# Performance work log

Measured on AMD Instinct MI355X. Metric: run time of the kernel, lower is better.

The kernel has to match this reference:

```python
import jax, jax.numpy as jnp
import numpy as np

N_NODES = 100000
N_EDGES = 1600000
F_IN_N = 64
F_IN_E = 64
F_OUT_N = 64
F_OUT_E = 64


def setup_inputs() -> dict:
    key = jax.random.key(0)
    ks = jax.random.split(key, 10)
    nfeats = jax.random.normal(ks[0], (N_NODES, F_IN_N), dtype=jnp.float32)
    efeats = jax.random.normal(ks[1], (N_EDGES, F_IN_E), dtype=jnp.float32)
    src = jax.random.randint(ks[2], (N_EDGES,), 0, N_NODES, dtype=jnp.int32)
    dst = jax.random.randint(ks[3], (N_EDGES,), 0, N_NODES, dtype=jnp.int32)
    s = 0.05
    W_node = jax.random.normal(ks[4], (F_OUT_N, F_IN_N), dtype=jnp.float32) * s
    b_node = jnp.zeros((F_OUT_N,), dtype=jnp.float32)
    W_ni = jax.random.normal(ks[5], (F_OUT_E, F_IN_N), dtype=jnp.float32) * s
    W_nj = jax.random.normal(ks[6], (F_OUT_E, F_IN_N), dtype=jnp.float32) * s
    W_fij = jax.random.normal(ks[7], (F_OUT_E, F_IN_E), dtype=jnp.float32) * s
    bias = jnp.zeros((F_OUT_E,), dtype=jnp.float32)
    return {"nfeats": nfeats, "efeats": efeats, "src": src, "dst": dst,
            "W_node": W_node, "b_node": b_node, "W_ni": W_ni, "W_nj": W_nj,
            "W_fij": W_fij, "bias": bias}


def reference(nfeats, efeats, src, dst, W_node, b_node, W_ni, W_nj, W_fij, bias):
    # edge update: leaky_relu(f_ni[src] + f_nj[dst] + f_fij + bias)
    f_ni = nfeats @ W_ni.T        # [N, Fe]
    f_nj = nfeats @ W_nj.T        # [N, Fe]
    f_fij = efeats @ W_fij.T      # [E, Fe]
    f_out = jax.nn.leaky_relu(f_ni[src] + f_nj[dst] + f_fij + bias, negative_slope=0.01)
    # node update: mean over in-edges of transformed source features
    h = nfeats @ W_node.T + b_node                      # [N, Fn]
    msg_sum = jax.ops.segment_sum(h[src], dst, num_segments=N_NODES)   # [N, Fn]
    deg = jax.ops.segment_sum(jnp.ones((src.shape[0],), dtype=h.dtype), dst,
                              num_segments=N_NODES)
    h_out = msg_sum / jnp.maximum(deg, 1.0)[:, None]    # 0 for isolated nodes
    return (h_out, f_out)
```

## Files before the change

kernel.cpp:

```cpp
#include <hip/hip_runtime.h>

#define NN 100000
#define NE 1600000
#define F 64
#define NSB ((NN + 255) / 256)
#define NTB ((NN + 127) / 128)

typedef float f32x4 __attribute__((ext_vector_type(4)));
typedef float f32x2 __attribute__((ext_vector_type(2)));
typedef short bf16x8 __attribute__((ext_vector_type(8)));

__device__ inline unsigned short f2bf(float f) {
    unsigned u = __builtin_bit_cast(unsigned, f);
    u = (u + 0x7fffu + ((u >> 16) & 1u)) >> 16;
    return (unsigned short)u;
}
__device__ inline float bf2f(unsigned short b) { return __builtin_bit_cast(float, (unsigned)b << 16); }
__device__ inline float bflo(unsigned u) { return __builtin_bit_cast(float, u << 16); }
__device__ inline float bfhi(unsigned u) { return __builtin_bit_cast(float, u & 0xffff0000u); }

__device__ inline bf16x8 pack8(const f32x4 v0, const f32x4 v1) {
    bf16x8 pk;
    pk[0] = (short)f2bf(v0[0]); pk[1] = (short)f2bf(v0[1]);
    pk[2] = (short)f2bf(v0[2]); pk[3] = (short)f2bf(v0[3]);
    pk[4] = (short)f2bf(v1[0]); pk[5] = (short)f2bf(v1[1]);
    pk[6] = (short)f2bf(v1[2]); pk[7] = (short)f2bf(v1[3]);
    return pk;
}

__global__ __launch_bounds__(256, 2) void node_kernel(
    const float* __restrict__ nfeats,
    const float* __restrict__ W_node, const float* __restrict__ b_node,
    const float* __restrict__ W_ni,   const float* __restrict__ W_nj,
    unsigned short* __restrict__ f_ni16, unsigned short* __restrict__ f_nj16,
    unsigned short* __restrict__ h16, int* __restrict__ counts)
{
    __shared__ bf16x8 As8[128 * 8];
    __shared__ bf16x8 Ws8[64 * 8];
    float* Df = reinterpret_cast<float*>(As8);

    const int t = threadIdx.x;
    const int w = t >> 6, lane = t & 63;
    const int tile0 = blockIdx.x * 128;
    const int m = blockIdx.y;

    if (m == 0 && t < 128 && tile0 + t < NN) counts[tile0 + t] = 0;

    {
        const float* Wp = (m == 0) ? W_ni : (m == 1) ? W_nj : W_node;
        const f32x4* gw = reinterpret_cast<const f32x4*>(Wp);
#pragma unroll
        for (int i = 0; i < 2; ++i) {
            const int c = i * 256 + t;
            const int row = c >> 3, slot = c & 7;
            Ws8[row * 8 + (slot ^ (row & 7))] = pack8(gw[2 * c], gw[2 * c + 1]);
        }
    }
    {
        const f32x4* gsrc = reinterpret_cast<const f32x4*>(nfeats + (size_t)tile0 * F);
#pragma unroll
        for (int i = 0; i < 4; ++i) {
            const int c = i * 256 + t;
            const int row = c >> 3, slot = c & 7;
            f32x4 v0 = f32x4{0.f, 0.f, 0.f, 0.f}, v1 = f32x4{0.f, 0.f, 0.f, 0.f};
            if (tile0 + row < NN) { v0 = gsrc[2 * c]; v1 = gsrc[2 * c + 1]; }
            As8[row * 8 + (slot ^ (row & 7))] = pack8(v0, v1);
        }
    }
    __syncthreads();

    bf16x8 af[2][2];
#pragma unroll
    for (int mt = 0; mt < 2; ++mt)
#pragma unroll
        for (int ks = 0; ks < 2; ++ks) {
            const int row = w * 32 + mt * 16 + (lane & 15);
            const int kslot = ks * 4 + (lane >> 4);
            af[mt][ks] = As8[row * 8 + (kslot ^ (row & 7))];
        }

    bf16x8 bfr[4][2];
#pragma unroll
    for (int nt = 0; nt < 4; ++nt)
#pragma unroll
        for (int ks = 0; ks < 2; ++ks) {
            const int c = nt * 16 + (lane & 15);
            const int kslot = ks * 4 + (lane >> 4);
            bfr[nt][ks] = Ws8[c * 8 + (kslot ^ (c & 7))];
        }

    f32x4 acc[2][4];
#pragma unroll
    for (int mt = 0; mt < 2; ++mt)
#pragma unroll
        for (int nt = 0; nt < 4; ++nt) acc[mt][nt] = f32x4{0.f, 0.f, 0.f, 0.f};
#pragma unroll
    for (int ks = 0; ks < 2; ++ks)
#pragma unroll
        for (int mt = 0; mt < 2; ++mt)
#pragma unroll
            for (int nt = 0; nt < 4; ++nt)
                acc[mt][nt] = __builtin_amdgcn_mfma_f32_16x16x32_bf16(
                    af[mt][ks], bfr[nt][ks], acc[mt][nt], 0, 0, 0);

    __syncthreads();

    unsigned short* outp = (m == 0) ? f_ni16 : (m == 1) ? f_nj16 : h16;

#pragma unroll
    for (int half = 0; half < 2; ++half) {
#pragma unroll
        for (int mt = 0; mt < 2; ++mt)
#pragma unroll
            for (int ntl = 0; ntl < 2; ++ntl) {
#pragma unroll
                for (int r = 0; r < 4; ++r) {
                    const int row = w * 32 + mt * 16 + (lane >> 4) * 4 + r;
                    const int col = ntl * 16 + (lane & 15);
                    float v = acc[mt][half * 2 + ntl][r];
                    if (m == 2) v += b_node[half * 32 + col];
                    Df[row * 32 + ((col + row) & 31)] = v;
                }
            }
        __syncthreads();

#pragma unroll
        for (int i = 0; i < 2; ++i) {
            const int idx = i * 256 + t;
            const int row = idx >> 2;
            const int c8 = (idx & 3) << 3;
            if (tile0 + row < NN) {
                const float* b = Df + row * 32;
                uint4 pk;
                unsigned u[4];
#pragma unroll
                for (int p = 0; p < 4; ++p) {
                    const unsigned lo = f2bf(b[(c8 + 2 * p + 0 + row) & 31]);
                    const unsigned hi = f2bf(b[(c8 + 2 * p + 1 + row) & 31]);
                    u[p] = lo | (hi << 16);
                }
                pk.x = u[0]; pk.y = u[1]; pk.z = u[2]; pk.w = u[3];
                *reinterpret_cast<uint4*>(outp + (size_t)(tile0 + row) * F + half * 32 + c8) = pk;
            }
        }
        __syncthreads();
    }
}

__global__ __launch_bounds__(256, 3) void edge_kernel(
    const float* __restrict__ efeats,
    const int* __restrict__ src, const int* __restrict__ dst,
    const unsigned short* __restrict__ f_ni16, const unsigned short* __restrict__ f_nj16,
    const float* __restrict__ W_fij, const float* __restrict__ bias,
    float* __restrict__ f_out, int* __restrict__ counts)
{
    __shared__ bf16x8 As8[256 * 8];
    __shared__ bf16x8 Ws8[64 * 8];
    float* Df = reinterpret_cast<float*>(As8);

    const int t = threadIdx.x;
    const int w = t >> 6, lane = t & 63;
    const int tile0 = blockIdx.x * 256;
    const int e = tile0 + t;
    const int s = src[e], d = dst[e];

    {
        const f32x4* gw = reinterpret_cast<const f32x4*>(W_fij);
#pragma unroll
        for (int i = 0; i < 2; ++i) {
            const int c = i * 256 + t;
            const int row = c >> 3, slot = c & 7;
            Ws8[row * 8 + (slot ^ (row & 7))] = pack8(gw[2 * c], gw[2 * c + 1]);
        }
    }
    {
        const f32x4* gsrc = reinterpret_cast<const f32x4*>(efeats + (size_t)tile0 * F);
#pragma unroll
        for (int i = 0; i < 8; ++i) {
            const int c = i * 256 + t;
            const int row = c >> 3, slot = c & 7;
            const f32x4 v0 = __builtin_nontemporal_load(gsrc + 2 * c);
            const f32x4 v1 = __builtin_nontemporal_load(gsrc + 2 * c + 1);
            As8[row * 8 + (slot ^ (row & 7))] = pack8(v0, v1);
        }
    }
    atomicAdd(&counts[d], 1);
    __syncthreads();

    bf16x8 af[4][2];
#pragma unroll
    for (int mt = 0; mt < 4; ++mt)
#pragma unroll
        for (int ks = 0; ks < 2; ++ks) {
            const int row = w * 64 + mt * 16 + (lane & 15);
            const int kslot = ks * 4 + (lane >> 4);
            af[mt][ks] = As8[row * 8 + (kslot ^ (row & 7))];
        }

    const uint4* gi = reinterpret_cast<const uint4*>(f_ni16 + (size_t)s * F);
    const uint4* gj = reinterpret_cast<const uint4*>(f_nj16 + (size_t)d * F);
    f32x4* gout = reinterpret_cast<f32x4*>(f_out + (size_t)tile0 * F);

#pragma unroll
    for (int half = 0; half < 2; ++half) {
        bf16x8 bfr[2][2];
#pragma unroll
        for (int ntl = 0; ntl < 2; ++ntl)
#pragma unroll
            for (int ks = 0; ks < 2; ++ks) {
                const int c = (half * 2 + ntl) * 16 + (lane & 15);
                const int kslot = ks * 4 + (lane >> 4);
                bfr[ntl][ks] = Ws8[c * 8 + (kslot ^ (c & 7))];
            }
        uint4 vni[4], vnj[4];
#pragma unroll
        for (int i = 0; i < 4; ++i) { vni[i] = gi[half * 4 + i]; vnj[i] = gj[half * 4 + i]; }

        f32x4 acc[4][2];
#pragma unroll
        for (int mt = 0; mt < 4; ++mt)
#pragma unroll
            for (int ntl = 0; ntl < 2; ++ntl) acc[mt][ntl] = f32x4{0.f, 0.f, 0.f, 0.f};
#pragma unroll
        for (int ks = 0; ks < 2; ++ks)
#pragma unroll
            for (int mt = 0; mt < 4; ++mt)
#pragma unroll
                for (int ntl = 0; ntl < 2; ++ntl)
                    acc[mt][ntl] = __builtin_amdgcn_mfma_f32_16x16x32_bf16(
                        af[mt][ks], bfr[ntl][ks], acc[mt][ntl], 0, 0, 0);

        __syncthreads();

#pragma unroll
        for (int mt = 0; mt < 4; ++mt)
#pragma unroll
            for (int ntl = 0; ntl < 2; ++ntl) {
#pragma unroll
                for (int r = 0; r < 4; ++r) {
                    const int row = w * 64 + mt * 16 + (lane >> 4) * 4 + r;
                    const int col = ntl * 16 + (lane & 15);
                    Df[row * 32 + ((col + row) & 31)] = acc[mt][ntl][r];
                }
            }
        __syncthreads();

        float* rb = Df + t * 32;
#pragma unroll
        for (int c = 0; c < 32; ++c) {
            float v = rb[(c + t) & 31];
            const unsigned wi = vni[c >> 3][(c >> 1) & 3];
            const unsigned wj = vnj[c >> 3][(c >> 1) & 3];
            v += (c & 1) ? bfhi(wi) : bflo(wi);
            v += (c & 1) ? bfhi(wj) : bflo(wj);
            v += bias[half * 32 + c];
            v = (v > 0.f) ? v : 0.01f * v;
            rb[(c + t) & 31] = v;
        }
        __syncthreads();

#pragma unroll
        for (int i = 0; i < 8; ++i) {
            const int idx = i * 256 + t;
            const int row = idx >> 3;
            const int c4 = (idx & 7) << 2;
            const float* b = Df + row * 32;
            f32x4 v;
            v[0] = b[(c4 + 0 + row) & 31];
            v[1] = b[(c4 + 1 + row) & 31];
            v[2] = b[(c4 + 2 + row) & 31];
            v[3] = b[(c4 + 3 + row) & 31];
            __builtin_nontemporal_store(v, gout + row * 16 + half * 8 + (idx & 7));
        }
        __syncthreads();
    }
}

__global__ __launch_bounds__(256) void scan1_kernel(
    const int* __restrict__ counts, int* __restrict__ offsets, int* __restrict__ blocksums)
{
    __shared__ int sd[256];
    const int t = threadIdx.x;
    const int i = blockIdx.x * 256 + t;
    const int v = (i < NN) ? counts[i] : 0;
    sd[t] = v;
    __syncthreads();
#pragma unroll
    for (int off = 1; off < 256; off <<= 1) {
        const int x = (t >= off) ? sd[t - off] : 0;
        __syncthreads();
        sd[t] += x;
        __syncthreads();
    }
    if (i < NN) offsets[i] = sd[t] - v;
    if (t == 255) blocksums[blockIdx.x] = sd[255];
}

__global__ __launch_bounds__(512) void scan2_kernel(
    const int* __restrict__ blocksums, int* __restrict__ blockpref)
{
    __shared__ int sd[512];
    const int t = threadIdx.x;
    const int v = (t < NSB) ? blocksums[t] : 0;
    sd[t] = v;
    __syncthreads();
#pragma unroll
    for (int off = 1; off < 512; off <<= 1) {
        const int x = (t >= off) ? sd[t - off] : 0;
        __syncthreads();
        sd[t] += x;
        __syncthreads();
    }
    if (t < NSB) blockpref[t] = sd[t] - v;
}

__global__ __launch_bounds__(256) void scan3_kernel(
    int* __restrict__ offsets, const int* __restrict__ blockpref, int* __restrict__ cursor)
{
    const int i = blockIdx.x * 256 + threadIdx.x;
    if (i < NN) {
        const int o = offsets[i] + blockpref[blockIdx.x];
        offsets[i] = o;
        cursor[i] = o;
    }
    if (i == 0) offsets[NN] = NE;
}

__global__ __launch_bounds__(256) void place_kernel(
    const int* __restrict__ src, const int* __restrict__ dst,
    int* __restrict__ cursor, int* __restrict__ eidx)
{
    const int e = blockIdx.x * 256 + threadIdx.x;
    if (e >= NE) return;
    const int pos = atomicAdd(&cursor[dst[e]], 1);
    eidx[pos] = src[e];
}

__global__ __launch_bounds__(256) void gather_kernel(
    const unsigned short* __restrict__ h16, const int* __restrict__ offsets,
    const int* __restrict__ eidx, float* __restrict__ h_out)
{
    const int n = blockIdx.x * 4 + (threadIdx.x >> 6);
    const int lane = threadIdx.x & 63;
    if (n >= NN) return;
    const int beg = offsets[n], end = offsets[n + 1];
    const int colp = (lane & 31) * 2;
    const int sel = lane >> 5;
    float a0 = 0.f, a1 = 0.f;
    int k = beg;
    for (; k + 4 <= end; k += 4) {
        const int e0 = eidx[k + sel];
        const int e1 = eidx[k + 2 + sel];
        const unsigned u0 = *reinterpret_cast<const unsigned*>(h16 + (size_t)e0 * F + colp);
        const unsigned u1 = *reinterpret_cast<const unsigned*>(h16 + (size_t)e1 * F + colp);
        a0 += bflo(u0) + bflo(u1);
        a1 += bfhi(u0) + bfhi(u1);
    }
    for (; k + 2 <= end; k += 2) {
        const int e0 = eidx[k + sel];
        const unsigned u0 = *reinterpret_cast<const unsigned*>(h16 + (size_t)e0 * F + colp);
        a0 += bflo(u0);
        a1 += bfhi(u0);
    }
    if (k < end && sel == 0) {
        const int e0 = eidx[k];
        const unsigned u0 = *reinterpret_cast<const unsigned*>(h16 + (size_t)e0 * F + colp);
        a0 += bflo(u0);
        a1 += bfhi(u0);
    }
    a0 += __shfl_xor(a0, 32, 64);
    a1 += __shfl_xor(a1, 32, 64);
    if (sel == 0) {
        const float dg = fmaxf((float)(end - beg), 1.0f);
        f32x2 o;
        o[0] = a0 / dg;
        o[1] = a1 / dg;
        __builtin_nontemporal_store(o, reinterpret_cast<f32x2*>(h_out + (size_t)n * F + colp));
    }
}

extern "C" void kernel_launch(void* const* d_in, const int* in_sizes, int n_in,
                              void* d_out, int out_size, void* d_ws, size_t ws_size,
                              hipStream_t stream)
{
    const float* nfeats = (const float*)d_in[0];
    const float* efeats = (const float*)d_in[1];
    const int*   src    = (const int*)  d_in[2];
    const int*   dst    = (const int*)  d_in[3];
    const float* W_node = (const float*)d_in[4];
    const float* b_node = (const float*)d_in[5];
    const float* W_ni   = (const float*)d_in[6];
    const float* W_nj   = (const float*)d_in[7];
    const float* W_fij  = (const float*)d_in[8];
    const float* bias   = (const float*)d_in[9];

    float* h_out = (float*)d_out;
    float* f_out = (float*)d_out + (size_t)NN * F;

    unsigned short* f_ni16 = (unsigned short*)d_ws;
    unsigned short* f_nj16 = f_ni16 + (size_t)NN * F;
    unsigned short* h16    = f_nj16 + (size_t)NN * F;
    int*   offsets = (int*)(h16 + (size_t)NN * F);
    int*   cursor  = offsets + (NN + 1);
    int*   counts  = cursor + NN;
    int*   eidx    = counts + NN;
    int*   blocksums = eidx + NE;
    int*   blockpref = blocksums + NSB;
    const size_t need = ((size_t)3 * NN * F) * sizeof(unsigned short)
                      + ((size_t)(3 * NN + 1) + NE + 2 * NSB) * sizeof(int);
    if (ws_size < need) return;

    node_kernel<<<dim3(NTB, 3), 256, 0, stream>>>(nfeats, W_node, b_node, W_ni, W_nj,
                                                  f_ni16, f_nj16, h16, counts);
    edge_kernel<<<NE / 256, 256, 0, stream>>>(efeats, src, dst, f_ni16, f_nj16, W_fij, bias,
                                              f_out, counts);
    scan1_kernel<<<NSB, 256, 0, stream>>>(counts, offsets, blocksums);
    scan2_kernel<<<1, 512, 0, stream>>>(blocksums, blockpref);
    scan3_kernel<<<NSB, 256, 0, stream>>>(offsets, blockpref, cursor);
    place_kernel<<<(NE + 255) / 256, 256, 0, stream>>>(src, dst, cursor, eidx);
    gather_kernel<<<(NN + 3) / 4, 256, 0, stream>>>(h16, offsets, eidx, h_out);
}
```

Measured before the change: 466.3 us.

## Fuse CSR placement into edge kernel and restructure epilogue into per-wave quarters

After: 473.3 us. No clear change (+1.5%).

```diff
diff --git a/kernel.cpp b/kernel.cpp
--- a/kernel.cpp
+++ b/kernel.cpp
@@ -28,12 +28,20 @@
     return pk;
 }
 
+__global__ __launch_bounds__(256) void hist_kernel(
+    const int* __restrict__ dst, int* __restrict__ counts)
+{
+    const int e = blockIdx.x * 256 + threadIdx.x;
+    if (e >= NE) return;
+    atomicAdd(&counts[dst[e]], 1);
+}
+
 __global__ __launch_bounds__(256, 2) void node_kernel(
     const float* __restrict__ nfeats,
     const float* __restrict__ W_node, const float* __restrict__ b_node,
     const float* __restrict__ W_ni,   const float* __restrict__ W_nj,
     unsigned short* __restrict__ f_ni16, unsigned short* __restrict__ f_nj16,
-    unsigned short* __restrict__ h16, int* __restrict__ counts)
+    unsigned short* __restrict__ h16)
 {
     __shared__ bf16x8 As8[128 * 8];
     __shared__ bf16x8 Ws8[64 * 8];
@@ -43,8 +51,6 @@
     const int w = t >> 6, lane = t & 63;
     const int tile0 = blockIdx.x * 128;
     const int m = blockIdx.y;
-
-    if (m == 0 && t < 128 && tile0 + t < NN) counts[tile0 + t] = 0;
 
     {
         const float* Wp = (m == 0) ? W_ni : (m == 1) ? W_nj : W_node;
@@ -147,12 +153,13 @@
     }
 }
 
-__global__ __launch_bounds__(256, 3) void edge_kernel(
+__global__ __launch_bounds__(256, 2) void edge_kernel(
     const float* __restrict__ efeats,
     const int* __restrict__ src, const int* __restrict__ dst,
     const unsigned short* __restrict__ f_ni16, const unsigned short* __restrict__ f_nj16,
     const float* __restrict__ W_fij, const float* __restrict__ bias,
-    float* __restrict__ f_out, int* __restrict__ counts)
+    float* __restrict__ f_out,
+    int* __restrict__ cursor, int* __restrict__ eidx)
 {
     __shared__ bf16x8 As8[256 * 8];
     __shared__ bf16x8 Ws8[64 * 8];
@@ -163,6 +170,18 @@
     const int tile0 = blockIdx.x * 256;
     const int e = tile0 + t;
     const int s = src[e], d = dst[e];
+
+    {
+        const int pos = atomicAdd(&cursor[d], 1);
+        eidx[pos] = s;
+    }
+
+    const uint4* gi = reinterpret_cast<const uint4*>(f_ni16 + (size_t)s * F);
+    const uint4* gj = reinterpret_cast<const uint4*>(f_nj16 + (size_t)d * F);
+
+    uint4 vni[2], vnj[2];
+#pragma unroll
+    for (int i = 0; i < 2; ++i) { vni[i] = gi[i]; vnj[i] = gj[i]; }
 
     {
         const f32x4* gw = reinterpret_cast<const f32x4*>(W_fij);
@@ -184,7 +203,6 @@
             As8[row * 8 + (slot ^ (row & 7))] = pack8(v0, v1);
         }
     }
-    atomicAdd(&counts[d], 1);
     __syncthreads();
 
     bf16x8 af[4][2];
@@ -196,83 +214,78 @@
             const int kslot = ks * 4 + (lane >> 4);
             af[mt][ks] = As8[row * 8 + (kslot ^ (row & 7))];
         }
-
-    const uint4* gi = reinterpret_cast<const uint4*>(f_ni16 + (size_t)s * F);
-    const uint4* gj = reinterpret_cast<const uint4*>(f_nj16 + (size_t)d * F);
+    __syncthreads();
+
     f32x4* gout = reinterpret_cast<f32x4*>(f_out + (size_t)tile0 * F);
 
 #pragma unroll
-    for (int half = 0; half < 2; ++half) {
-        bf16x8 bfr[2][2];
-#pragma unroll
-        for (int ntl = 0; ntl < 2; ++ntl)
-#pragma unroll
-            for (int ks = 0; ks < 2; ++ks) {
-                const int c = (half * 2 + ntl) * 16 + (lane & 15);
-                const int kslot = ks * 4 + (lane >> 4);
-                bfr[ntl][ks] = Ws8[c * 8 + (kslot ^ (c & 7))];
+    for (int q = 0; q < 4; ++q) {
+        bf16x8 bfr[2];
+#pragma unroll
+        for (int ks = 0; ks < 2; ++ks) {
+            const int c = q * 16 + (lane & 15);
+            const int kslot = ks * 4 + (lane >> 4);
+            bfr[ks] = Ws8[c * 8 + (kslot ^ (c & 7))];
+        }
+        f32x4 acc[4];
+#pragma unroll
+        for (int mt = 0; mt < 4; ++mt) acc[mt] = f32x4{0.f, 0.f, 0.f, 0.f};
+#pragma unroll
+        for (int ks = 0; ks < 2; ++ks)
+#pragma unroll
+            for (int mt = 0; mt < 4; ++mt)
+                acc[mt] = __builtin_amdgcn_mfma_f32_16x16x32_bf16(
+                    af[mt][ks], bfr[ks], acc[mt], 0, 0, 0);
+
+        uint4 nni[2], nnj[2];
+        if (q < 3) {
+#pragma unroll
+            for (int i = 0; i < 2; ++i) { nni[i] = gi[2 * (q + 1) + i]; nnj[i] = gj[2 * (q + 1) + i]; }
+        }
+
+#pragma unroll
+        for (int mt = 0; mt < 4; ++mt)
+#pragma unroll
+            for (int r = 0; r < 4; ++r) {
+                const int row = w * 64 + mt * 16 + (lane >> 4) * 4 + r;
+                const int col = lane & 15;
+                Df[row * 16 + ((col + row) & 15)] = acc[mt][r];
             }
-        uint4 vni[4], vnj[4];
-#pragma unroll
-        for (int i = 0; i < 4; ++i) { vni[i] = gi[half * 4 + i]; vnj[i] = gj[half * 4 + i]; }
-
-        f32x4 acc[4][2];
-#pragma unroll
-        for (int mt = 0; mt < 4; ++mt)
-#pragma unroll
-            for (int ntl = 0; ntl < 2; ++ntl) acc[mt][ntl] = f32x4{0.f, 0.f, 0.f, 0.f};
-#pragma unroll
-        for (int ks = 0; ks < 2; ++ks)
-#pragma unroll
-            for (int mt = 0; mt < 4; ++mt)
-#pragma unroll
-                for (int ntl = 0; ntl < 2; ++ntl)
-                    acc[mt][ntl] = __builtin_amdgcn_mfma_f32_16x16x32_bf16(
-                        af[mt][ks], bfr[ntl][ks], acc[mt][ntl], 0, 0, 0);
-
-        __syncthreads();
-
-#pragma unroll
-        for (int mt = 0; mt < 4; ++mt)
-#pragma unroll
-            for (int ntl = 0; ntl < 2; ++ntl) {
-#pragma unroll
-                for (int r = 0; r < 4; ++r) {
-                    const int row = w * 64 + mt * 16 + (lane >> 4) * 4 + r;
-                    const int col = ntl * 16 + (lane & 15);
-                    Df[row * 32 + ((col + row) & 31)] = acc[mt][ntl][r];
-                }
+        __builtin_amdgcn_wave_barrier();
+
+        {
+            float* rb = Df + t * 16;
+#pragma unroll
+            for (int c = 0; c < 16; ++c) {
+                float v = rb[(c + t) & 15];
+                const unsigned wi = vni[c >> 3][(c >> 1) & 3];
+                const unsigned wj = vnj[c >> 3][(c >> 1) & 3];
+                v += (c & 1) ? bfhi(wi) : bflo(wi);
+                v += (c & 1) ? bfhi(wj) : bflo(wj);
+                v += bias[q * 16 + c];
+                v = (v > 0.f) ? v : 0.01f * v;
+                rb[(c + t) & 15] = v;
             }
-        __syncthreads();
-
-        float* rb = Df + t * 32;
-#pragma unroll
-        for (int c = 0; c < 32; ++c) {
-            float v = rb[(c + t) & 31];
-            const unsigned wi = vni[c >> 3][(c >> 1) & 3];
-            const unsigned wj = vnj[c >> 3][(c >> 1) & 3];
-            v += (c & 1) ? bfhi(wi) : bflo(wi);
-            v += (c & 1) ? bfhi(wj) : bflo(wj);
-            v += bias[half * 32 + c];
-            v = (v > 0.f) ? v : 0.01f * v;
-            rb[(c + t) & 31] = v;
-        }
-        __syncthreads();
-
-#pragma unroll
-        for (int i = 0; i < 8; ++i) {
-            const int idx = i * 256 + t;
-            const int row = idx >> 3;
-            const int c4 = (idx & 7) << 2;
-            const float* b = Df + row * 32;
+        }
+        __builtin_amdgcn_wave_barrier();
+
+#pragma unroll
+        for (int i = 0; i < 4; ++i) {
+            const int idx = i * 64 + lane;
+            const int row = w * 64 + (idx >> 2);
+            const int c4 = (idx & 3) << 2;
+            const float* b = Df + row * 16;
             f32x4 v;
-            v[0] = b[(c4 + 0 + row) & 31];
-            v[1] = b[(c4 + 1 + row) & 31];
-            v[2] = b[(c4 + 2 + row) & 31];
-            v[3] = b[(c4 + 3 + row) & 31];
-            __builtin_nontemporal_store(v, gout + row * 16 + half * 8 + (idx & 7));
-        }
-        __syncthreads();
+            v[0] = b[(c4 + 0 + row) & 15];
+            v[1] = b[(c4 + 1 + row) & 15];
+            v[2] = b[(c4 + 2 + row) & 15];
+            v[3] = b[(c4 + 3 + row) & 15];
+            __builtin_nontemporal_store(v, gout + row * 16 + q * 4 + (idx & 3));
+        }
+        __builtin_amdgcn_wave_barrier();
+
+#pragma unroll
+        for (int i = 0; i < 2; ++i) { vni[i] = nni[i]; vnj[i] = nnj[i]; }
     }
 }
 
@@ -324,16 +337,6 @@
         cursor[i] = o;
     }
     if (i == 0) offsets[NN] = NE;
-}
-
-__global__ __launch_bounds__(256) void place_kernel(
-    const int* __restrict__ src, const int* __restrict__ dst,
-    int* __restrict__ cursor, int* __restrict__ eidx)
-{
-    const int e = blockIdx.x * 256 + threadIdx.x;
-    if (e >= NE) return;
-    const int pos = atomicAdd(&cursor[dst[e]], 1);
-    eidx[pos] = src[e];
 }
 
 __global__ __launch_bounds__(256) void gather_kernel(
@@ -410,13 +413,15 @@
                       + ((size_t)(3 * NN + 1) + NE + 2 * NSB) * sizeof(int);
     if (ws_size < need) return;
 
-    node_kernel<<<dim3(NTB, 3), 256, 0, stream>>>(nfeats, W_node, b_node, W_ni, W_nj,
-                                                  f_ni16, f_nj16, h16, counts);
-    edge_kernel<<<NE / 256, 256, 0, stream>>>(efeats, src, dst, f_ni16, f_nj16, W_fij, bias,
-                                              f_out, counts);
+    hipMemsetAsync(counts, 0, (size_t)NN * sizeof(int), stream);
+
+    hist_kernel<<<(NE + 255) / 256, 256, 0, stream>>>(dst, counts);
     scan1_kernel<<<NSB, 256, 0, stream>>>(counts, offsets, blocksums);
     scan2_kernel<<<1, 512, 0, stream>>>(blocksums, blockpref);
     scan3_kernel<<<NSB, 256, 0, stream>>>(offsets, blockpref, cursor);
-    place_kernel<<<(NE + 255) / 256, 256, 0, stream>>>(src, dst, cursor, eidx);
+    node_kernel<<<dim3(NTB, 3), 256, 0, stream>>>(nfeats, W_node, b_node, W_ni, W_nj,
+                                                  f_ni16, f_nj16, h16);
+    edge_kernel<<<NE / 256, 256, 0, stream>>>(efeats, src, dst, f_ni16, f_nj16, W_fij, bias,
+                                              f_out, cursor, eidx);
     gather_kernel<<<(NN + 3) / 4, 256, 0, stream>>>(h16, offsets, eidx, h_out);
 }
```
